# Performance work log

Hardware: AMD Instinct MI355X
Metric: run time of the kernel (lower is better)

Reference implementation:

```python
import jax, jax.numpy as jnp
import numpy as np

KSIZE, SCALE, STRIDE, SOFTMAX_SCALE = 3, 3, 1, 10.0
ESCAPE_NAN = 1e-4
DN = ('NCHW', 'OIHW', 'NCHW')


def same_pad(x, k, stride):
    # torch same_padding: pad so out = ceil(in/stride)
    H, W = x.shape[-2], x.shape[-1]
    oh, ow = -(-H // stride), -(-W // stride)
    ph = max(0, (oh - 1) * stride + k - H)
    pw = max(0, (ow - 1) * stride + k - W)
    return jnp.pad(x, ((0, 0), (0, 0), (ph // 2, ph - ph // 2), (pw // 2, pw - pw // 2)))


def extract_patches(img, k, stride):
    # img [B,C,H,W] already padded -> [B, L, C, k, k], matching torch Unfold ordering (C slowest, kh, kw)
    B, C, H, W = img.shape
    oh, ow = (H - k) // stride + 1, (W - k) // stride + 1
    cols = [img[:, :, i:i + stride * oh:stride, j:j + stride * ow:stride]
            for i in range(k) for j in range(k)]
    p = jnp.stack(cols, axis=2)                      # [B, C, k*k, oh, ow]
    p = p.reshape(B, C, k, k, oh * ow)               # [B, C, k, k, L]
    return jnp.transpose(p, (0, 4, 1, 2, 3))         # [B, L, C, k, k]


def conv1x1_prelu(x, W, b, a):
    y = jnp.einsum('bchw,oc->bohw', x, W) + b[None, :, None, None]
    return jnp.where(y >= 0, y, a * y)


def bilinear_down(x, Ho, Wo):
    # F.interpolate(mode='bilinear', align_corners=False), no antialias
    H, W = x.shape[-2], x.shape[-1]
    def coords(o, s):
        src = (jnp.arange(o, dtype=jnp.float32) + 0.5) * (s / o) - 0.5
        src = jnp.clip(src, 0.0, s - 1.0)
        i0 = jnp.floor(src).astype(jnp.int32)
        i1 = jnp.minimum(i0 + 1, s - 1)
        return i0, i1, src - i0.astype(jnp.float32)
    y0, y1, wy = coords(Ho, H)
    x0, x1, wx = coords(Wo, W)
    r = x[:, :, y0, :] * (1.0 - wy)[:, None] + x[:, :, y1, :] * wy[:, None]
    return r[:, :, :, x0] * (1.0 - wx) + r[:, :, :, x1] * wx


def forward(x, Wa, ba, aa, Wm1, bm1, am1, Wm2, bm2, am2):
    B, C, H, W = x.shape
    kernel = SCALE * KSIZE  # 9
    embed_w = conv1x1_prelu(x, Wa, ba, aa)      # [B,C,H,W]
    match = conv1x1_prelu(x, Wm1, bm1, am1)     # [B,C/2,H,W]
    # large-scale patches used as conv_transpose kernels: [B, L, C, 9, 9]
    raw_w = extract_patches(same_pad(embed_w, kernel, STRIDE * SCALE), kernel, STRIDE * SCALE)
    Hr, Wr = H // SCALE, W // SCALE
    ref = conv1x1_prelu(bilinear_down(x, Hr, Wr), Wm2, bm2, am2)  # [B,C/2,Hr,Wr]
    # small-scale patches used as correlation kernels: [B, L, C/2, 3, 3]
    w = extract_patches(same_pad(ref, KSIZE, STRIDE), KSIZE, STRIDE)
    norm = jnp.sqrt(jnp.sum(w * w, axis=(2, 3, 4), keepdims=True))
    wn = w / jnp.maximum(norm, ESCAPE_NAN)
    xp = same_pad(match, KSIZE, 1)  # [B,C/2,H+2,W+2]

    def corr(xi, wi):  # xi [C/2,H+2,W+2], wi [L,C/2,3,3] -> [L,H,W]
        return jax.lax.conv_general_dilated(xi[None], wi, (1, 1), 'VALID', dimension_numbers=DN)[0]

    y = jax.vmap(corr)(xp, wn)                  # [B,L,H,W]
    y = jax.nn.softmax(y * SOFTMAX_SCALE, axis=1)

    pad = kernel - 1 - SCALE  # conv_transpose2d(stride=3, padding=3) equivalent padding = 5

    def tconv(yi, rwi):  # yi [L,H,W], rwi [L,C,9,9] -> [C,3H,3W]
        k = jnp.transpose(jnp.flip(rwi, (-2, -1)), (1, 0, 2, 3))  # [C,L,9,9]
        return jax.lax.conv_general_dilated(
            yi[None], k, (1, 1), [(pad, pad), (pad, pad)],
            lhs_dilation=(STRIDE * SCALE, STRIDE * SCALE), dimension_numbers=DN)[0]

    out = jax.vmap(tconv)(y, raw_w) / 6.0       # [B,C,3H,3W]
    return out


def setup_inputs() -> dict:
    key = jax.random.key(0)
    ks = jax.random.split(key, 8)
    B, C, H, W = 4, 64, 60, 60
    C2 = C // 2
    return {
        'x': jax.random.normal(ks[0], (B, C, H, W), jnp.float32),
        'Wa': jax.random.normal(ks[1], (C, C), jnp.float32) * 0.1,
        'ba': jax.random.normal(ks[2], (C,), jnp.float32) * 0.1,
        'aa': jnp.full((1,), 0.25, jnp.float32),
        'Wm1': jax.random.normal(ks[3], (C2, C), jnp.float32) * 0.1,
        'bm1': jax.random.normal(ks[4], (C2,), jnp.float32) * 0.1,
        'am1': jnp.full((1,), 0.25, jnp.float32),
        'Wm2': jax.random.normal(ks[5], (C2, C), jnp.float32) * 0.1,
        'bm2': jax.random.normal(ks[6], (C2,), jnp.float32) * 0.1,
        'am2': jnp.full((1,), 0.25, jnp.float32),
    }


def reference(x, Wa, ba, aa, Wm1, bm1, am1, Wm2, bm2, am2):
    return forward(x, Wa, ba, aa, Wm1, bm1, am1, Wm2, bm2, am2)
```

## Files before the change

### kernel.cpp

```cpp
#include <hip/hip_runtime.h>
#include <hip/hip_bf16.h>

typedef __hip_bfloat16 bf16_t;
using f32x4  = __attribute__((ext_vector_type(4))) float;
using bf16x8 = __attribute__((ext_vector_type(8))) short;

#define NB 4
#define NC 64
#define NC2 32
#define NH 60
#define NW 60
#define NPIX (NH*NW)
#define HP 66
#define MP 62
#define HR 20
#define RP 22
#define NL 400
#define OHW 180
#define KPAD 512

#define OFF_XPB   2230272
#define OFF_REFP  3214336
#define OFF_YBL   3462144
#define OFF_AP    14982144
#define OFF_EB    29727744
#define OFF_XP    32087040
#define OFF_RF    40381440

__global__ __launch_bounds__(256) void k_conv(
    const float* __restrict__ x,
    const float* __restrict__ Wa,  const float* __restrict__ ba,  const float* __restrict__ aa,
    const float* __restrict__ Wm1, const float* __restrict__ bm1, const float* __restrict__ am1,
    const float* __restrict__ Wm2, const float* __restrict__ bm2, const float* __restrict__ am2,
    bf16_t* __restrict__ E_bt, bf16_t* __restrict__ xpb, float* __restrict__ refp) {
  int bid = blockIdx.x;
  int t = threadIdx.x;
  if (bid < 300) {
    __shared__ float Ws[64*64];
    __shared__ float bs[64];
    __shared__ float al;
    int b = bid / 75, pblk = bid % 75;
    for (int i = t; i < 64*64; i += 256) {
      int co = i >> 6, c = i & 63;
      Ws[c*64 + co] = Wa[i];
    }
    if (t < 64) bs[t] = ba[t];
    if (t == 0) al = aa[0];
    __syncthreads();
    int lane = t & 63, wid = t >> 6;
    int pix0 = pblk*48 + wid*12;
    const float* xb = x + b*NC*NPIX + pix0;
    float acc[12];
    #pragma unroll
    for (int p = 0; p < 12; ++p) acc[p] = bs[lane];
    for (int c = 0; c < 64; ++c) {
      float wv = Ws[c*64 + lane];
      const float* xc = xb + c*NPIX;
      #pragma unroll
      for (int p = 0; p < 12; ++p)
        acc[p] = fmaf(xc[p], wv, acc[p]);
    }
    #pragma unroll
    for (int p = 0; p < 12; ++p) {
      float v = acc[p];
      v = v >= 0.f ? v : al*v;
      int pix = pix0 + p;
      int ph = pix / NW, pw = pix % NW;
      E_bt[((b*HP + ph+3)*HP + (pw+3))*NC + lane] = __float2bfloat16(v);
    }
  } else if (bid < 2100) {
    int idx = (bid - 300)*256 + t;
    int pix = idx % NPIX; int tmp = idx / NPIX;
    int co = tmp % NC2; int b = tmp / NC2;
    float alpha = am1[0];
    const float* xb = x + b*NC*NPIX + pix;
    const float* wr = Wm1 + co*64;
    float acc = bm1[co];
    #pragma unroll 8
    for (int c = 0; c < 64; ++c)
      acc = fmaf(xb[c*NPIX], wr[c], acc);
    acc = acc >= 0.f ? acc : alpha*acc;
    int ph = pix / NW, pw = pix % NW;
    xpb[((b*NC2 + co)*MP + ph+1)*MP + (pw+1)] = __float2bfloat16(acc);
  } else if (bid < 2300) {
    int idx = (bid - 2100)*256 + t;
    int pos = idx % (HR*HR); int tmp = idx / (HR*HR);
    int co = tmp % NC2; int b = tmp / NC2;
    int hr = pos / HR, wr_ = pos % HR;
    float alpha = am2[0];
    const float* xb = x + b*NC*NPIX + (3*hr+1)*NW + (3*wr_+1);
    const float* wrow = Wm2 + co*64;
    float acc = bm2[co];
    #pragma unroll 8
    for (int c = 0; c < 64; ++c)
      acc = fmaf(xb[c*NPIX], wrow[c], acc);
    acc = acc >= 0.f ? acc : alpha*acc;
    refp[((b*NC2 + co)*RP + hr+1)*RP + (wr_+1)] = acc;
  } else {
    unsigned short* Eu = (unsigned short*)E_bt;
    unsigned short* Xu = (unsigned short*)xpb;
    int g0 = (bid - 2300)*256 + t;
    for (int g = g0; g < 235520; g += 80*256) {
      if (g < 193536) {
        int b = g / 48384, e = g % 48384;
        int addr;
        if (e < 25344) {
          int r6 = e / 4224, off = e % 4224;
          int ph = (r6 < 3) ? r6 : 60 + r6;
          addr = (b*HP + ph)*4224 + off;
        } else {
          int e2 = e - 25344;
          int row = e2 / 384, off2 = e2 % 384;
          int pos = (off2 < 192) ? off2 : 4032 + (off2 - 192);
          addr = (b*HP + 3 + row)*4224 + pos;
        }
        Eu[addr] = 0;
      } else if (g < 224768) {
        int gg = g - 193536;
        int p = gg / 244, e = gg % 244;
        int pos;
        if (e < 62) pos = e;
        else if (e < 124) pos = 3782 + (e - 62);
        else { int i = e - 124; pos = (1 + (i >> 1))*62 + (i & 1)*61; }
        Xu[p*3844 + pos] = 0;
      } else {
        int gg = g - 224768;
        int p = gg / 84, e = gg % 84;
        int pos;
        if (e < 22) pos = e;
        else if (e < 44) pos = 462 + (e - 22);
        else { int i = e - 44; pos = (1 + (i >> 1))*22 + (i & 1)*21; }
        refp[p*484 + pos] = 0.f;
      }
    }
  }
}

__global__ __launch_bounds__(256) void k_swz(
    const bf16_t* __restrict__ xpb, const float* __restrict__ refp,
    const bf16_t* __restrict__ E_bt,
    bf16_t* __restrict__ Xp, bf16_t* __restrict__ Rf, bf16_t* __restrict__ Eb) {
  __shared__ float scl[16];
  int bid = blockIdx.x;
  int t = threadIdx.x;
  if (bid < 2025) {
    int tid = bid*256 + t;
    int slot = tid & 63; int rest = tid >> 6;
    int ks = rest % 9; int rest2 = rest / 9;
    int mblk = rest2 % 225; int b = rest2 / 225;
    int m = mblk*16 + (slot & 15);
    int h = m / NW, w = m % NW;
    int k0 = ks*32 + (slot >> 4)*8;
    const bf16_t* xb = xpb + (size_t)b*NC2*MP*MP;
    union { bf16_t a[8]; bf16x8 v; } u;
    #pragma unroll
    for (int j = 0; j < 8; ++j) {
      int k = k0 + j;
      int c = k / 9, r = k % 9;
      int i = r / 3, j2 = r % 3;
      u.a[j] = xb[(c*MP + h + i)*MP + w + j2];
    }
    *(bf16x8*)(Xp + (size_t)tid*8) = u.v;
  } else if (bid < 2125) {
    int r2 = bid - 2025;
    int nblk = r2 % 25, b = r2 / 25;
    int ll = t >> 4, sub = t & 15;
    int l = nblk*16 + ll;
    int lh = l / HR, lw = l % HR;
    const float* rb = refp + (size_t)b*NC2*RP*RP;
    float ss = 0.f;
    #pragma unroll
    for (int e0 = 0; e0 < 18; ++e0) {
      int e = sub*18 + e0;
      int c = e / 9, r = e % 9;
      int i = r / 3, j = r % 3;
      float v = rb[(c*RP + lh + i)*RP + lw + j];
      ss = fmaf(v, v, ss);
    }
    #pragma unroll
    for (int off = 1; off < 16; off <<= 1)
      ss += __shfl_xor(ss, off);
    if (sub == 0) scl[ll] = 10.f / fmaxf(sqrtf(ss), 1e-4f);
    __syncthreads();
    for (int sidx = t; sidx < 576; sidx += 256) {
      int ks = sidx >> 6, slot = sidx & 63;
      int l2 = nblk*16 + (slot & 15);
      int lh2 = l2 / HR, lw2 = l2 % HR;
      float sc = scl[slot & 15];
      int k0 = ks*32 + (slot >> 4)*8;
      union { bf16_t a[8]; bf16x8 v; } u;
      #pragma unroll
      for (int j = 0; j < 8; ++j) {
        int k = k0 + j;
        int c = k / 9, r = k % 9;
        int i = r / 3, j2 = r % 3;
        u.a[j] = __float2bfloat16(rb[(c*RP + lh2 + i)*RP + lw2 + j2] * sc);
      }
      *(bf16x8*)(Rf + ((size_t)(b*25 + nblk)*576 + sidx)*8) = u.v;
    }
  } else {
    int r2 = bid - 2125;
    int n = r2 % 576, b = r2 / 576;
    int c = n / 9, n9 = n % 9, rr = n9 / 3, s = n9 % 3;
    size_t nbase = ((size_t)(b*12 + n/48)*16);
    const unsigned short* Eu = (const unsigned short*)E_bt;
    unsigned short* Ebu = (unsigned short*)Eb;
    for (int k = t; k < KPAD; k += 256) {
      unsigned short v = 0;
      if (k < 484) {
        int u = k / 22, vv = k % 22;
        v = Eu[((size_t)((b*HP + 3*u + rr)*HP + 3*vv + s))*NC + c];
      }
      size_t idx = (((nbase + (k>>5))*3 + (n%48)/16)*64 + ((k>>3)&3)*16 + (n&15))*8 + (k&7);
      Ebu[idx] = v;
    }
  }
}

__global__ __launch_bounds__(64) void k_cgemm(
    const bf16x8* __restrict__ Xp, const bf16x8* __restrict__ Rf,
    bf16_t* __restrict__ y_bl) {
  __shared__ __align__(16) bf16_t ytile[48][80];
  int L = threadIdx.x;
  int o = blockIdx.x;
  int xcd = o & 7, sl = o >> 3;
  int w = (xcd < 4 ? xcd*188 : 752 + (xcd-4)*187) + sl;
  int b = w / 375; int rem = w % 375;
  int mt = rem / 5, nt = rem % 5;
  const bf16x8* pa = Xp + ((size_t)(b*225 + mt*3)*9)*64 + L;
  const bf16x8* pb = Rf + ((size_t)(b*25 + nt*5)*9)*64 + L;
  f32x4 acc[3][5];
  #pragma unroll
  for (int i = 0; i < 3; ++i)
    #pragma unroll
    for (int j = 0; j < 5; ++j)
      acc[i][j] = {0.f, 0.f, 0.f, 0.f};
  bf16x8 A[3][3], B[3][5];
  #pragma unroll
  for (int i = 0; i < 3; ++i) { A[0][i] = pa[i*576]; A[1][i] = pa[i*576 + 64]; }
  #pragma unroll
  for (int j = 0; j < 5; ++j) { B[0][j] = pb[j*576]; B[1][j] = pb[j*576 + 64]; }
  #pragma unroll
  for (int ks = 0; ks < 9; ++ks) {
    if (ks < 7) {
      #pragma unroll
      for (int i = 0; i < 3; ++i) A[(ks+2)%3][i] = pa[i*576 + (ks+2)*64];
      #pragma unroll
      for (int j = 0; j < 5; ++j) B[(ks+2)%3][j] = pb[j*576 + (ks+2)*64];
    }
    #pragma unroll
    for (int i = 0; i < 3; ++i)
      #pragma unroll
      for (int j = 0; j < 5; ++j)
        acc[i][j] = __builtin_amdgcn_mfma_f32_16x16x32_bf16(A[ks%3][i], B[ks%3][j], acc[i][j], 0, 0, 0);
  }
  int quad = L >> 4, col = L & 15;
  #pragma unroll
  for (int mf = 0; mf < 3; ++mf)
    #pragma unroll
    for (int r = 0; r < 4; ++r)
      #pragma unroll
      for (int nf = 0; nf < 5; ++nf)
        ytile[mf*16 + quad*4 + r][nf*16 + col] = __float2bfloat16(acc[mf][nf][r]);
  __syncthreads();
  bf16_t* dst0 = y_bl + ((size_t)(b*NPIX + mt*48))*NL + nt*80;
  for (int i = L; i < 480; i += 64) {
    int row = i / 10, seg = i % 10;
    *(bf16x8*)(dst0 + (size_t)row*NL + seg*8) = *(const bf16x8*)&ytile[row][seg*8];
  }
}

__device__ __forceinline__ float lo_bf(unsigned int u) {
  return __uint_as_float(u << 16);
}
__device__ __forceinline__ float hi_bf(unsigned int u) {
  return __uint_as_float(u & 0xffff0000u);
}
__device__ __forceinline__ float u16_bf(unsigned short u) {
  return __uint_as_float(((unsigned int)u) << 16);
}
__device__ __forceinline__ unsigned short bf_bits(float f) {
  union { bf16_t h; unsigned short u; } c;
  c.h = __float2bfloat16(f);
  return c.u;
}

__global__ __launch_bounds__(512) void k_saprime(
    const unsigned int* __restrict__ y_b32, bf16_t* __restrict__ Ap) {
  __shared__ uint4 raw[2592];
  unsigned short* ysp = (unsigned short*)raw;
  int t = threadIdx.x;
  int b = blockIdx.z;
  int h0base = blockIdx.y*4, w0base = blockIdx.x*4;
  for (int i = t; i < 2592; i += 512) raw[i] = uint4{0,0,0,0};
  __syncthreads();

  int wave = t >> 6, lane = t & 63;
  bool act = lane < 50;
  for (int pos = wave; pos < 36; pos += 8) {
    int i = pos / 6, jj = pos % 6;
    int hh = h0base - 1 + i, ww = w0base - 1 + jj;
    if (!((unsigned)hh < NH && (unsigned)ww < NW)) continue;
    const uint4* src4 = (const uint4*)(y_b32 + ((size_t)(b*NPIX + hh*NW + ww))*200);
    uint4 v = act ? src4[lane] : uint4{0,0,0,0};
    float f[8];
    if (act) {
      f[0] = lo_bf(v.x); f[1] = hi_bf(v.x);
      f[2] = lo_bf(v.y); f[3] = hi_bf(v.y);
      f[4] = lo_bf(v.z); f[5] = hi_bf(v.z);
      f[6] = lo_bf(v.w); f[7] = hi_bf(v.w);
    } else {
      #pragma unroll
      for (int k = 0; k < 8; ++k) f[k] = -1e30f;
    }
    float m = -1e30f;
    #pragma unroll
    for (int k = 0; k < 8; ++k) m = fmaxf(m, f[k]);
    #pragma unroll
    for (int off = 32; off > 0; off >>= 1)
      m = fmaxf(m, __shfl_xor(m, off));
    float s = 0.f;
    #pragma unroll
    for (int k = 0; k < 8; ++k) {
      float e = __expf(f[k] - m);
      f[k] = e;
      s += e;
    }
    #pragma unroll
    for (int off = 32; off > 0; off >>= 1)
      s += __shfl_xor(s, off);
    float r = 1.f / s;
    if (act) {
      #pragma unroll
      for (int k = 0; k < 4; ++k) {
        int l2 = lane*4 + k;
        int lh = l2 / 10, lw = 2*l2 - 20*lh;
        union { bf16_t h[2]; unsigned int u; } pk;
        pk.h[0] = __float2bfloat16(f[2*k]   * r);
        pk.h[1] = __float2bfloat16(f[2*k+1] * r);
        *(unsigned int*)&ysp[pos*576 + (lh+2)*24 + (lw+2)] = pk.u;
      }
    }
  }
  __syncthreads();

  int row = t >> 5;
  int klane = t & 31;
  int h0r = row >> 2, w0r = row & 3;
  int m = (h0base + h0r)*NW + (w0base + w0r);
  int pblk = m / 80, pf = (m % 80) >> 4, mrow = m & 15;
  size_t rowbase = ((size_t)(b*45 + pblk)*16);
  const unsigned short* basep = ysp + (h0r*6 + w0r)*576;
  unsigned short* Apu = (unsigned short*)Ap;
  for (int kk = 0; kk < 8; ++kk) {
    int k = kk*64 + 2*klane;
    float a0 = 0.f, a1 = 0.f;
    if (k < 484) {
      int u = k / 22, v = k - 22*u;
      const unsigned short* q = basep + u*24 + v;
      #pragma unroll
      for (int dh = 0; dh < 3; ++dh) {
        unsigned int p0 = *(const unsigned int*)(q + dh*3480);
        a0 += lo_bf(p0); a1 += hi_bf(p0);
        a0 += u16_bf(q[dh*3480 + 577]);
        a1 += u16_bf(q[dh*3480 + 578]);
        unsigned int p2 = *(const unsigned int*)(q + dh*3480 + 1154);
        a0 += lo_bf(p2); a1 += hi_bf(p2);
      }
    }
    unsigned int pk = ((unsigned int)bf_bits(a1) << 16) | bf_bits(a0);
    size_t idx = (((rowbase + (k>>5))*5 + pf)*64 + ((k>>3)&3)*16 + mrow)*8 + (k&7);
    *(unsigned int*)&Apu[idx] = pk;
  }
}

__global__ __launch_bounds__(64) void k_tgemm(
    const bf16x8* __restrict__ Eb, const bf16x8* __restrict__ Ap,
    float* __restrict__ out) {
  __shared__ __align__(16) float otile[80][52];
  int L = threadIdx.x;
  int o = blockIdx.x;
  int w = (o & 7)*270 + (o >> 3);
  int b = w / 540; int rem = w % 540;
  int pbi = rem / 12, rb = rem % 12;
  const bf16x8* pa = Eb + ((size_t)(b*12 + rb)*16)*3*64 + L;
  const bf16x8* pp = Ap + ((size_t)(b*45 + pbi)*16)*5*64 + L;
  f32x4 acc[3][5];
  #pragma unroll
  for (int i = 0; i < 3; ++i)
    #pragma unroll
    for (int j = 0; j < 5; ++j)
      acc[i][j] = {0.f, 0.f, 0.f, 0.f};
  bf16x8 A[3][3], B[3][5];
  #pragma unroll
  for (int i = 0; i < 3; ++i) { A[0][i] = pa[i*64]; A[1][i] = pa[192 + i*64]; }
  #pragma unroll
  for (int j = 0; j < 5; ++j) { B[0][j] = pp[j*64]; B[1][j] = pp[320 + j*64]; }
  #pragma unroll
  for (int ks = 0; ks < 16; ++ks) {
    if (ks < 14) {
      const bf16x8* na = pa + (ks+2)*192;
      const bf16x8* nb = pp + (ks+2)*320;
      #pragma unroll
      for (int i = 0; i < 3; ++i) A[(ks+2)%3][i] = na[i*64];
      #pragma unroll
      for (int j = 0; j < 5; ++j) B[(ks+2)%3][j] = nb[j*64];
    }
    #pragma unroll
    for (int i = 0; i < 3; ++i)
      #pragma unroll
      for (int j = 0; j < 5; ++j)
        acc[i][j] = __builtin_amdgcn_mfma_f32_16x16x32_bf16(A[ks%3][i], B[ks%3][j], acc[i][j], 0, 0, 0);
  }
  int quad = L >> 4, col = L & 15;
  const float sc = 1.f/6.f;
  #pragma unroll
  for (int pf = 0; pf < 5; ++pf)
    #pragma unroll
    for (int rf = 0; rf < 3; ++rf) {
      f32x4 v = acc[rf][pf];
      v[0] *= sc; v[1] *= sc; v[2] *= sc; v[3] *= sc;
      *(f32x4*)&otile[pf*16 + col][rf*16 + quad*4] = v;
    }
  __syncthreads();
  if (L < 60) {
    float* ob = out + b*(NC*OHW*OHW);
    int m0 = pbi*80;
    int f0 = 4*L;
    int mi0 = f0/3,     s0 = f0 - 3*mi0;
    int mi1 = (f0+1)/3, s1 = (f0+1) - 3*mi1;
    int mi2 = (f0+2)/3, s2 = (f0+2) - 3*mi2;
    int mi3 = (f0+3)/3, s3 = (f0+3) - 3*mi3;
    int m  = m0 + mi0;
    int h0 = m / 60, w0 = m - 60*h0;
    int lane_off = (3*h0)*180 + 3*w0 + s0;
    const float* g0 = &otile[mi0][s0];
    const float* g1 = &otile[mi1][s1];
    const float* g2 = &otile[mi2][s2];
    const float* g3 = &otile[mi3][s3];
    int rb3 = rb % 3;
    int cc = (rb*48)/9;
    int rr = rb3;
    #pragma unroll
    for (int p = 0; p < 16; ++p) {
      f32x4 v;
      v[0] = g0[p*3];
      v[1] = g1[p*3];
      v[2] = g2[p*3];
      v[3] = g3[p*3];
      *(f32x4*)&ob[cc*32400 + rr*180 + lane_off] = v;
      ++rr; if (rr == 3) { rr = 0; ++cc; }
    }
  }
}

extern "C" void kernel_launch(void* const* d_in, const int* in_sizes, int n_in,
                              void* d_out, int out_size, void* d_ws, size_t ws_size,
                              hipStream_t stream) {
  (void)in_sizes; (void)n_in; (void)out_size; (void)ws_size;
  const float* x   = (const float*)d_in[0];
  const float* Wa  = (const float*)d_in[1];
  const float* ba  = (const float*)d_in[2];
  const float* aa  = (const float*)d_in[3];
  const float* Wm1 = (const float*)d_in[4];
  const float* bm1 = (const float*)d_in[5];
  const float* am1 = (const float*)d_in[6];
  const float* Wm2 = (const float*)d_in[7];
  const float* bm2 = (const float*)d_in[8];
  const float* am2 = (const float*)d_in[9];
  float* out = (float*)d_out;

  char* base = (char*)d_ws;
  bf16_t* E_bt  = (bf16_t*)base;
  bf16_t* xpb   = (bf16_t*)(base + OFF_XPB);
  float*  refp  = (float*)(base + OFF_REFP);
  bf16_t* y_bl  = (bf16_t*)(base + OFF_YBL);
  bf16_t* ApSwz = (bf16_t*)(base + OFF_AP);
  bf16_t* EbSwz = (bf16_t*)(base + OFF_EB);
  bf16_t* XpSwz = (bf16_t*)(base + OFF_XP);
  bf16_t* RfSwz = (bf16_t*)(base + OFF_RF);

  k_conv<<<2380, 256, 0, stream>>>(x, Wa, ba, aa, Wm1, bm1, am1, Wm2, bm2, am2,
                                   E_bt, xpb, refp);
  k_swz<<<4429, 256, 0, stream>>>(xpb, refp, E_bt, XpSwz, RfSwz, EbSwz);
  k_cgemm<<<1500, 64, 0, stream>>>((const bf16x8*)XpSwz, (const bf16x8*)RfSwz, y_bl);
  k_saprime<<<dim3(15, 15, NB), 512, 0, stream>>>((const unsigned int*)y_bl, ApSwz);
  k_tgemm<<<2160, 64, 0, stream>>>((const bf16x8*)EbSwz, (const bf16x8*)ApSwz, out);
}
```

Before: 163.7 us.

## Stream tgemm operands through LDS ring with direct global-to-LDS loads

Replaces the register triple-buffered operand prefetch in the transposed-conv GEMM with a 4-deep LDS ring filled by global_load_lds (direct global-to-shared) instructions. Manual vmcnt waits keep up to three stages of loads in flight while MFMAs run on the current stage. The aim is deeper memory latency hiding and lower register pressure, at the cost of extra LDS reads and hand-tuned wait counts that must match the load count exactly.

```diff
diff --git a/kernel.cpp b/kernel.cpp
--- a/kernel.cpp
+++ b/kernel.cpp
@@ -374,9 +374,16 @@
   }
 }
 
+__device__ __forceinline__ void gload_lds16(const bf16x8* g, bf16x8* l) {
+  __builtin_amdgcn_global_load_lds(
+      (const __attribute__((address_space(1))) unsigned int*)g,
+      (__attribute__((address_space(3))) unsigned int*)l, 16, 0, 0);
+}
+
 __global__ __launch_bounds__(64) void k_tgemm(
     const bf16x8* __restrict__ Eb, const bf16x8* __restrict__ Ap,
     float* __restrict__ out) {
+  __shared__ __align__(16) bf16x8 ring[4][8][64];
   __shared__ __align__(16) float otile[80][52];
   int L = threadIdx.x;
   int o = blockIdx.x;
@@ -391,26 +398,39 @@
     #pragma unroll
     for (int j = 0; j < 5; ++j)
       acc[i][j] = {0.f, 0.f, 0.f, 0.f};
-  bf16x8 A[3][3], B[3][5];
-  #pragma unroll
-  for (int i = 0; i < 3; ++i) { A[0][i] = pa[i*64]; A[1][i] = pa[192 + i*64]; }
-  #pragma unroll
-  for (int j = 0; j < 5; ++j) { B[0][j] = pp[j*64]; B[1][j] = pp[320 + j*64]; }
+  #pragma unroll
+  for (int d = 0; d < 4; ++d) {
+    #pragma unroll
+    for (int i = 0; i < 3; ++i) gload_lds16(pa + d*192 + i*64, &ring[d][i][0]);
+    #pragma unroll
+    for (int j = 0; j < 5; ++j) gload_lds16(pp + d*320 + j*64, &ring[d][3+j][0]);
+  }
   #pragma unroll
   for (int ks = 0; ks < 16; ++ks) {
-    if (ks < 14) {
-      const bf16x8* na = pa + (ks+2)*192;
-      const bf16x8* nb = pp + (ks+2)*320;
-      #pragma unroll
-      for (int i = 0; i < 3; ++i) A[(ks+2)%3][i] = na[i*64];
-      #pragma unroll
-      for (int j = 0; j < 5; ++j) B[(ks+2)%3][j] = nb[j*64];
-    }
+    if (ks < 13)      asm volatile("s_waitcnt vmcnt(24)" ::: "memory");
+    else if (ks == 13) asm volatile("s_waitcnt vmcnt(16)" ::: "memory");
+    else if (ks == 14) asm volatile("s_waitcnt vmcnt(8)"  ::: "memory");
+    else               asm volatile("s_waitcnt vmcnt(0)"  ::: "memory");
+    bf16x8 af[3], bf[5];
+    #pragma unroll
+    for (int i = 0; i < 3; ++i) af[i] = ring[ks & 3][i][L];
+    #pragma unroll
+    for (int j = 0; j < 5; ++j) bf[j] = ring[ks & 3][3+j][L];
+    asm volatile("s_waitcnt lgkmcnt(0)" ::: "memory");
+    __builtin_amdgcn_sched_barrier(0);
+    if (ks + 4 < 16) {
+      int d = ks + 4;
+      #pragma unroll
+      for (int i = 0; i < 3; ++i) gload_lds16(pa + d*192 + i*64, &ring[d & 3][i][0]);
+      #pragma unroll
+      for (int j = 0; j < 5; ++j) gload_lds16(pp + d*320 + j*64, &ring[d & 3][3+j][0]);
+    }
+    __builtin_amdgcn_sched_barrier(0);
     #pragma unroll
     for (int i = 0; i < 3; ++i)
       #pragma unroll
       for (int j = 0; j < 5; ++j)
-        acc[i][j] = __builtin_amdgcn_mfma_f32_16x16x32_bf16(A[ks%3][i], B[ks%3][j], acc[i][j], 0, 0, 0);
+        acc[i][j] = __builtin_amdgcn_mfma_f32_16x16x32_bf16(af[i], bf[j], acc[i][j], 0, 0, 0);
   }
   int quad = L >> 4, col = L & 15;
   const float sc = 1.f/6.f;
```

New measurement: 166.5 us. About the same (+1.7%).
